# Performance work log

Measured on AMD Instinct MI355X. Metric: run time of the kernel, lower is better.

The kernel has to match this reference:

```python
import jax, jax.numpy as jnp
import numpy as np

L, H, LATENT, DM, DH, FF = 4, 4, 256, 768, 192, 1024
EPS = 1e-6      # fast_transformers RecurrentLinearAttention eps
LN_EPS = 1e-5


def make_pe(d_model=LATENT, max_len=5000):
    pos = np.arange(max_len, dtype=np.float32)[:, None]
    div = np.exp(np.arange(0, d_model, 2, dtype=np.float32) * (-np.log(10000.0) / d_model))
    pe = np.zeros((max_len, d_model), np.float32)
    pe[:, 0::2] = np.sin(pos * div)
    pe[:, 1::2] = np.cos(pos * div)
    return jnp.asarray(pe)

PE = make_pe()


def layer_norm(x, g, b):
    m = x.mean(-1, keepdims=True)
    v = ((x - m) ** 2).mean(-1, keepdims=True)
    return (x - m) * jax.lax.rsqrt(v + LN_EPS) * g + b


def setup_inputs() -> dict:
    key = jax.random.key(0)
    ks = jax.random.split(key, 16)
    bs, nj, nf, T, A, C = 8, 25, 6, 80, 6, 12
    s = 0.02
    return dict(
        x=jax.random.normal(ks[0], (bs, nj, nf, T), jnp.float32),
        y=jax.random.randint(ks[1], (bs, A), 0, C),
        ind_map=jnp.sort(jax.random.randint(ks[2], (T, bs), 0, A), axis=0),
        act_tstamps=jnp.sort(jax.random.randint(ks[3], (bs, A), 1, T + 1), axis=1).at[:, -1].set(T),
        skel_W=jax.random.normal(ks[4], (nj * nf, LATENT), jnp.float32) * s,
        skel_b=jnp.zeros((LATENT,), jnp.float32),
        muQuery=jax.random.normal(ks[5], (C, LATENT), jnp.float32),
        sigmaQuery=jax.random.normal(ks[6], (C, LATENT), jnp.float32),
        Wq=jax.random.normal(ks[7], (L, DM, DM), jnp.float32) * s,
        bq=jnp.zeros((L, DM), jnp.float32),
        Wk=jax.random.normal(ks[8], (L, DM, DM), jnp.float32) * s,
        bk=jnp.zeros((L, DM), jnp.float32),
        Wv=jax.random.normal(ks[9], (L, DM, DM), jnp.float32) * s,
        bv=jnp.zeros((L, DM), jnp.float32),
        Wo=jax.random.normal(ks[10], (L, DM, DM), jnp.float32) * s,
        bo=jnp.zeros((L, DM), jnp.float32),
        W1=jax.random.normal(ks[11], (L, DM, FF), jnp.float32) * s,
        b1=jnp.zeros((L, FF), jnp.float32),
        W2=jax.random.normal(ks[12], (L, FF, DM), jnp.float32) * s,
        b2=jnp.zeros((L, DM), jnp.float32),
        ln1_g=jnp.ones((L, DM), jnp.float32), ln1_b=jnp.zeros((L, DM), jnp.float32),
        ln2_g=jnp.ones((L, DM), jnp.float32), ln2_b=jnp.zeros((L, DM), jnp.float32),
        lnf_g=jnp.ones((DM,), jnp.float32), lnf_b=jnp.zeros((DM,), jnp.float32),
    )


def _fwd(x, y, ind_map, act_tstamps, skel_W, skel_b, muQuery, sigmaQuery,
         Wq, bq, Wk, bk, Wv, bv, Wo, bo, W1, b1, W2, b2,
         ln1_g, ln1_b, ln2_g, ln2_b, lnf_g, lnf_b):
    bs, nj, nf, T = x.shape
    # skeleton embedding: [T, bs, njoints*nfeats] @ W -> [T, bs, LATENT]
    xe = x.transpose(3, 0, 1, 2).reshape(T, bs, nj * nf) @ skel_W + skel_b
    mu_q = muQuery[y]        # [bs, A, LATENT]
    sig_q = sigmaQuery[y]
    barange = jnp.arange(bs)

    @jax.checkpoint
    def step(carry, inputs):
        S, Z = carry                         # [L,bs,H,DH,DH], [L,bs,H,DH]
        t, xt, ind_t = inputs
        cm = mu_q[barange, ind_t]            # gather per-sample current action query
        cs = sig_q[barange, ind_t]
        xseq = jnp.stack([cm, cs, xt], 0)    # [3, bs, LATENT]
        start = jnp.where(t == 0, 0, t + 2)  # PositionalEncoding(last_pos=t, offset=2)
        pe3 = jax.lax.dynamic_slice_in_dim(PE, start, 3, 0)
        xseq = xseq + pe3[:, None, :]
        h = xseq.transpose(1, 0, 2).reshape(bs, 3 * LATENT)  # flatten -> [bs, DM]
        nS, nZ = [], []
        for l in range(L):
            q = (h @ Wq[l] + bq[l]).reshape(bs, H, DH)
            k = (h @ Wk[l] + bk[l]).reshape(bs, H, DH)
            v = (h @ Wv[l] + bv[l]).reshape(bs, H, DH)
            Q = jax.nn.elu(q) + 1.0          # linear-attention feature map
            K = jax.nn.elu(k) + 1.0
            Sl = S[l] + K[..., :, None] * v[..., None, :]   # state update S += k (x) v
            Zl = Z[l] + K
            inv = 1.0 / (jnp.einsum('bhd,bhd->bh', Q, Zl) + EPS)
            att = jnp.einsum('bhd,bhdm,bh->bhm', Q, Sl, inv).reshape(bs, DM)
            h1 = layer_norm(h + att @ Wo[l] + bo[l], ln1_g[l], ln1_b[l])
            ffn = jax.nn.relu(h1 @ W1[l] + b1[l]) @ W2[l] + b2[l]
            h = layer_norm(h1 + ffn, ln2_g[l], ln2_b[l])
            nS.append(Sl); nZ.append(Zl)
        h = layer_norm(h, lnf_g, lnf_b)      # encoder final norm
        return (jnp.stack(nS), jnp.stack(nZ)), h

    S0 = jnp.zeros((L, bs, H, DH, DH), x.dtype)
    Z0 = jnp.zeros((L, bs, H, DH), x.dtype)
    _, finals = jax.lax.scan(step, (S0, Z0), (jnp.arange(T), xe, ind_map))  # finals: [T,bs,DM]
    tsel = jnp.maximum(act_tstamps - 1, 0)                       # [bs, A]
    mu = finals[:, :, :LATENT][tsel, barange[:, None]]           # [bs, A, LATENT]
    logvar = finals[:, :, LATENT:2 * LATENT][tsel, barange[:, None]]
    return mu, logvar


def reference(x, y, ind_map, act_tstamps, skel_W, skel_b, muQuery, sigmaQuery,
              Wq, bq, Wk, bk, Wv, bv, Wo, bo, W1, b1, W2, b2,
              ln1_g, ln1_b, ln2_g, ln2_b, lnf_g, lnf_b):
    return _fwd(x, y, ind_map, act_tstamps, skel_W, skel_b, muQuery, sigmaQuery,
                Wq, bq, Wk, bk, Wv, bv, Wo, bo, W1, b1, W2, b2,
                ln1_g, ln1_b, ln2_g, ln2_b, lnf_g, lnf_b)
```

## Files before the change

kernel.cpp:

```cpp
#include <hip/hip_runtime.h>
#include <math.h>

#define TT 80
#define BS 8
#define NA 6
#define DMODEL 768
#define NH 4
#define DH 192
#define FFD 1024
#define NROWS (TT*BS)
#define NQKV (3*DMODEL)

typedef __bf16 bf16;
typedef __bf16 bf16x8 __attribute__((ext_vector_type(8)));
typedef float  f32x4  __attribute__((ext_vector_type(4)));

__device__ __forceinline__ float block_reduce_sum256(float v, float* sm4) {
#pragma unroll
    for (int off = 32; off > 0; off >>= 1) v += __shfl_down(v, off, 64);
    int lane = threadIdx.x & 63, wid = threadIdx.x >> 6;
    if (lane == 0) sm4[wid] = v;
    __syncthreads();
    float r = sm4[0] + sm4[1] + sm4[2] + sm4[3];
    __syncthreads();
    return r;
}

__global__ __launch_bounds__(256) void embed_k(
        const float* __restrict__ x, const int* __restrict__ y,
        const int* __restrict__ ind_map, const float* __restrict__ skel_W,
        const float* __restrict__ skel_b, const float* __restrict__ muQ,
        const float* __restrict__ sigQ, float* __restrict__ h0,
        bf16* __restrict__ h0b) {
    __shared__ float xrow[152];
    int r = blockIdx.x;
    int t = r >> 3, b = r & 7;
    int c = threadIdx.x;
    if (c < 150) xrow[c] = x[(b * 150 + c) * TT + t];
    __syncthreads();
    float acc = skel_b[c];
    for (int jf = 0; jf < 150; jf++) acc += xrow[jf] * skel_W[jf * 256 + c];
    int ind_t = ind_map[t * 8 + b];
    int yb = y[b * NA + ind_t];
    float cm = muQ[yb * 256 + c];
    float cs = sigQ[yb * 256 + c];
    int start = (t == 0) ? 0 : (t + 2);
    float div = expf((float)(c & ~1) * (-9.210340371976184f / 256.0f));
    float p0, p1, p2;
    if (c & 1) {
        p0 = cosf((float)start * div);
        p1 = cosf((float)(start + 1) * div);
        p2 = cosf((float)(start + 2) * div);
    } else {
        p0 = sinf((float)start * div);
        p1 = sinf((float)(start + 1) * div);
        p2 = sinf((float)(start + 2) * div);
    }
    float* hr = h0 + (size_t)r * DMODEL;
    float v0 = cm + p0, v1 = cs + p1, v2 = acc + p2;
    hr[c] = v0; hr[c + 256] = v1; hr[c + 512] = v2;
    bf16* hb = h0b + (size_t)r * DMODEL;
    hb[c] = (bf16)v0; hb[c + 256] = (bf16)v1; hb[c + 512] = (bf16)v2;
}

__global__ __launch_bounds__(256) void transpose_k(
        const float* __restrict__ Wq, const float* __restrict__ Wk,
        const float* __restrict__ Wv, const float* __restrict__ Wo,
        const float* __restrict__ W1, const float* __restrict__ W2,
        bf16* __restrict__ qkvT, bf16* __restrict__ woT,
        bf16* __restrict__ w1T, bf16* __restrict__ w2T) {
    int lz = blockIdx.z;
    int l = lz >> 2, z = lz & 3;
    int K = (z == 3) ? 1024 : 768;
    int N = (z == 0) ? 2304 : (z == 2) ? 1024 : 768;
    int k0 = blockIdx.x * 32, n0 = blockIdx.y * 32;
    if (k0 >= K || n0 >= N) return;
    const float* src; bf16* dst; int ldsrc; int ncol;
    if (z == 0) {
        if (n0 < 768)       { src = Wq + (size_t)l * 768 * 768; ncol = n0; }
        else if (n0 < 1536) { src = Wk + (size_t)l * 768 * 768; ncol = n0 - 768; }
        else                { src = Wv + (size_t)l * 768 * 768; ncol = n0 - 1536; }
        dst = qkvT + (size_t)l * NQKV * DMODEL; ldsrc = 768;
    } else if (z == 1) { src = Wo + (size_t)l * 768 * 768;  dst = woT + (size_t)l * 768 * 768;  ldsrc = 768;  ncol = n0; }
    else if (z == 2)   { src = W1 + (size_t)l * 768 * 1024; dst = w1T + (size_t)l * 1024 * 768; ldsrc = 1024; ncol = n0; }
    else               { src = W2 + (size_t)l * 1024 * 768; dst = w2T + (size_t)l * 768 * 1024; ldsrc = 768;  ncol = n0; }
    __shared__ float tile[32][33];
    int tx = threadIdx.x & 31, ty = threadIdx.x >> 5;
#pragma unroll
    for (int i = 0; i < 4; i++) {
        int r = ty + 8 * i;
        tile[r][tx] = src[(size_t)(k0 + r) * ldsrc + ncol + tx];
    }
    __syncthreads();
#pragma unroll
    for (int i = 0; i < 4; i++) {
        int r = ty + 8 * i;
        dst[(size_t)(n0 + r) * K + k0 + tx] = (bf16)tile[tx][r];
    }
}

template <int EPI>
__global__ __launch_bounds__(256) void gemm_mfma(
        const bf16* __restrict__ A, const bf16* __restrict__ Bt,
        const float* __restrict__ bias_q, const float* __restrict__ bias_k,
        const float* __restrict__ bias_v, const float* __restrict__ resid,
        float* __restrict__ outF, bf16* __restrict__ outB,
        int M, int N, int K) {
    __shared__ __attribute__((aligned(16))) bf16 As0[64][40];
    __shared__ __attribute__((aligned(16))) bf16 As1[64][40];
    __shared__ __attribute__((aligned(16))) bf16 Bs0[64][40];
    __shared__ __attribute__((aligned(16))) bf16 Bs1[64][40];
    int tid = threadIdx.x;
    int m0 = blockIdx.y * 64, n0 = blockIdx.x * 64;
    int w = tid >> 6;
    int l = tid & 63;
    int lm = l & 15, lq = l >> 4;
    int sr = tid >> 2;
    int sk = (tid & 3) * 8;
    const bf16* Arow = &A[(size_t)(m0 + sr) * K];
    const bf16* Brow = &Bt[(size_t)(n0 + sr) * K];
    f32x4 acc[4] = {};
    uint4 a0 = *(const uint4*)&Arow[sk];
    uint4 a1 = *(const uint4*)&Arow[32 + sk];
    uint4 b0 = *(const uint4*)&Brow[sk];
    uint4 b1 = *(const uint4*)&Brow[32 + sk];
    for (int k0 = 0; k0 < K; k0 += 64) {
        __syncthreads();
        *(uint4*)&As0[sr][sk] = a0;
        *(uint4*)&As1[sr][sk] = a1;
        *(uint4*)&Bs0[sr][sk] = b0;
        *(uint4*)&Bs1[sr][sk] = b1;
        __syncthreads();
        int k2 = k0 + 64; if (k2 >= K) k2 = 0;
        a0 = *(const uint4*)&Arow[k2 + sk];
        a1 = *(const uint4*)&Arow[k2 + 32 + sk];
        b0 = *(const uint4*)&Brow[k2 + sk];
        b1 = *(const uint4*)&Brow[k2 + 32 + sk];
        bf16x8 af0 = *(bf16x8*)&As0[w * 16 + lm][lq * 8];
        bf16x8 af1 = *(bf16x8*)&As1[w * 16 + lm][lq * 8];
#pragma unroll
        for (int nb = 0; nb < 4; nb++) {
            bf16x8 bf0 = *(bf16x8*)&Bs0[nb * 16 + lm][lq * 8];
            acc[nb] = __builtin_amdgcn_mfma_f32_16x16x32_bf16(af0, bf0, acc[nb], 0, 0, 0);
        }
#pragma unroll
        for (int nb = 0; nb < 4; nb++) {
            bf16x8 bf1 = *(bf16x8*)&Bs1[nb * 16 + lm][lq * 8];
            acc[nb] = __builtin_amdgcn_mfma_f32_16x16x32_bf16(af1, bf1, acc[nb], 0, 0, 0);
        }
    }
#pragma unroll
    for (int nb = 0; nb < 4; nb++) {
        int col = n0 + nb * 16 + lm;
        float b;
        bool do_elu = false;
        if (EPI == 0) {
            if (col < 768)       { b = bias_q[col];        do_elu = true; }
            else if (col < 1536) { b = bias_k[col - 768];  do_elu = true; }
            else                 { b = bias_v[col - 1536]; }
        } else {
            b = bias_q[col];
        }
#pragma unroll
        for (int r = 0; r < 4; r++) {
            int row = m0 + w * 16 + lq * 4 + r;
            float v = acc[nb][r] + b;
            if (EPI == 0) {
                if (do_elu) v = (v > 0.0f) ? (v + 1.0f) : expf(v);
                outB[(size_t)row * N + col] = (bf16)v;
            } else if (EPI == 1) {
                v += resid[(size_t)row * N + col];
                outF[(size_t)row * N + col] = v;
            } else {
                v = fmaxf(v, 0.0f);
                outB[(size_t)row * N + col] = (bf16)v;
            }
        }
    }
}

__global__ __launch_bounds__(256) void ln_k(
        const float* __restrict__ in, float* __restrict__ outF,
        bf16* __restrict__ outB,
        const float* __restrict__ g, const float* __restrict__ b) {
    int wave = threadIdx.x >> 6, lane = threadIdx.x & 63;
    int row = blockIdx.x * 4 + wave;
    const float* xr = in + (size_t)row * DMODEL;
    float4 v[3];
    float s = 0.0f;
#pragma unroll
    for (int j = 0; j < 3; j++) {
        v[j] = *(const float4*)&xr[lane * 4 + 256 * j];
        s += v[j].x + v[j].y + v[j].z + v[j].w;
    }
#pragma unroll
    for (int mk = 1; mk < 64; mk <<= 1) s += __shfl_xor(s, mk, 64);
    float m = s * (1.0f / 768.0f);
    float sq = 0.0f;
#pragma unroll
    for (int j = 0; j < 3; j++) {
        v[j].x -= m; v[j].y -= m; v[j].z -= m; v[j].w -= m;
        sq += v[j].x * v[j].x + v[j].y * v[j].y + v[j].z * v[j].z + v[j].w * v[j].w;
    }
#pragma unroll
    for (int mk = 1; mk < 64; mk <<= 1) sq += __shfl_xor(sq, mk, 64);
    float r = rsqrtf(sq * (1.0f / 768.0f) + 1e-5f);
    float* orow = outF + (size_t)row * DMODEL;
    bf16* brow = outB + (size_t)row * DMODEL;
#pragma unroll
    for (int j = 0; j < 3; j++) {
        int c = lane * 4 + 256 * j;
        float4 gg = *(const float4*)&g[c];
        float4 bb = *(const float4*)&b[c];
        float o0 = v[j].x * r * gg.x + bb.x;
        float o1 = v[j].y * r * gg.y + bb.y;
        float o2 = v[j].z * r * gg.z + bb.z;
        float o3 = v[j].w * r * gg.w + bb.w;
        *(float4*)&orow[c] = make_float4(o0, o1, o2, o3);
        bf16 tmp4[4] = {(bf16)o0, (bf16)o1, (bf16)o2, (bf16)o3};
        *(uint2*)&brow[c] = *(uint2*)tmp4;
    }
}

__global__ __launch_bounds__(320) void attn_k(
        const bf16* __restrict__ qkvB, bf16* __restrict__ att) {
    __shared__ __attribute__((aligned(16))) char smem[64000];
    bf16* Qs = (bf16*)smem;
    bf16* Ks = (bf16*)(smem + 32000);
    bf16* Aij = (bf16*)smem;
    bf16* VT = (bf16*)(smem + 16640);

    int b = blockIdx.x >> 2, h = blockIdx.x & 3;
    int tid = threadIdx.x;
    int w = tid >> 6, l = tid & 63;
    int lm = l & 15, lq = l >> 4;

    uint4 vreg[6];
#pragma unroll
    for (int u = 0; u < 6; u++) {
        int c = tid + 320 * u;
        int t = c / 24, cc = c % 24;
        int d0 = cc * 8;
        size_t g = (size_t)(t * 8 + b) * NQKV + h * DH + d0;
        uint4 qv = *(const uint4*)&qkvB[g];
        uint4 kv = *(const uint4*)&qkvB[g + 768];
        vreg[u]  = *(const uint4*)&qkvB[g + 1536];
        *(uint4*)&Qs[t * 200 + d0] = qv;
        *(uint4*)&Ks[t * 200 + d0] = kv;
    }
    __syncthreads();

    f32x4 acc[5] = {};
#pragma unroll
    for (int k0 = 0; k0 < 192; k0 += 32) {
        bf16x8 af = *(bf16x8*)&Qs[(w * 16 + lm) * 200 + lq * 8 + k0];
#pragma unroll
        for (int nb = 0; nb < 5; nb++) {
            bf16x8 bfr = *(bf16x8*)&Ks[(nb * 16 + lm) * 200 + lq * 8 + k0];
            acc[nb] = __builtin_amdgcn_mfma_f32_16x16x32_bf16(af, bfr, acc[nb], 0, 0, 0);
        }
    }
    float mval[5][4];
    float rs[4] = {0.f, 0.f, 0.f, 0.f};
#pragma unroll
    for (int nb = 0; nb < 5; nb++)
#pragma unroll
        for (int r = 0; r < 4; r++) {
            int t = w * 16 + lq * 4 + r, tau = nb * 16 + lm;
            float v = (tau <= t) ? acc[nb][r] : 0.0f;
            mval[nb][r] = v;
            rs[r] += v;
        }
#pragma unroll
    for (int mk = 1; mk < 16; mk <<= 1)
#pragma unroll
        for (int r = 0; r < 4; r++) rs[r] += __shfl_xor(rs[r], mk, 64);
    float inv[4];
#pragma unroll
    for (int r = 0; r < 4; r++) inv[r] = 1.0f / (rs[r] + 1e-6f);

    __syncthreads();

#pragma unroll
    for (int nb = 0; nb < 5; nb++)
#pragma unroll
        for (int r = 0; r < 4; r++)
            Aij[(w * 16 + lq * 4 + r) * 104 + nb * 16 + lm] = (bf16)mval[nb][r];
    *(uint2*)&Aij[(tid >> 2) * 104 + 80 + (tid & 3) * 4] = make_uint2(0u, 0u);
#pragma unroll
    for (int u = 0; u < 6; u++) {
        int c = tid + 320 * u;
        int t = c / 24, cc = c % 24;
        int d0 = cc * 8;
        bf16 tmp8[8];
        *(uint4*)tmp8 = vreg[u];
#pragma unroll
        for (int j = 0; j < 8; j++) VT[(d0 + j) * 104 + t] = tmp8[j];
    }
    if (tid < 192) {
        *(uint4*)&VT[tid * 104 + 80] = make_uint4(0u, 0u, 0u, 0u);
        *(uint4*)&VT[tid * 104 + 88] = make_uint4(0u, 0u, 0u, 0u);
    }
    __syncthreads();

#pragma unroll 1
    for (int nc = 0; nc < 12; nc++) {
        f32x4 a2 = {};
#pragma unroll
        for (int k0 = 0; k0 < 96; k0 += 32) {
            bf16x8 af = *(bf16x8*)&Aij[(w * 16 + lm) * 104 + lq * 8 + k0];
            bf16x8 bfr = *(bf16x8*)&VT[(nc * 16 + lm) * 104 + lq * 8 + k0];
            a2 = __builtin_amdgcn_mfma_f32_16x16x32_bf16(af, bfr, a2, 0, 0, 0);
        }
#pragma unroll
        for (int r = 0; r < 4; r++) {
            int t = w * 16 + lq * 4 + r;
            att[(size_t)(t * 8 + b) * DMODEL + h * DH + nc * 16 + lm] =
                (bf16)(a2[r] * inv[r]);
        }
    }
}

__global__ __launch_bounds__(256) void final_k(
        const float* __restrict__ h, const int* __restrict__ act_ts,
        const float* __restrict__ g, const float* __restrict__ bb,
        float* __restrict__ out) {
    __shared__ float sm4[4];
    int ba = blockIdx.x;
    int b = ba / NA;
    int ts = act_ts[ba];
    int t = ts - 1; if (t < 0) t = 0;
    const float* xr = h + (size_t)(t * 8 + b) * DMODEL;
    int c = threadIdx.x;
    float x0 = xr[c], x1 = xr[c + 256], x2 = xr[c + 512];
    float m = block_reduce_sum256(x0 + x1 + x2, sm4) * (1.0f / 768.0f);
    float d0 = x0 - m, d1 = x1 - m, d2 = x2 - m;
    float v = block_reduce_sum256(d0 * d0 + d1 * d1 + d2 * d2, sm4) * (1.0f / 768.0f);
    float r = rsqrtf(v + 1e-5f);
    out[ba * 256 + c]            = d0 * r * g[c] + bb[c];
    out[48 * 256 + ba * 256 + c] = d1 * r * g[c + 256] + bb[c + 256];
}

extern "C" void kernel_launch(void* const* d_in, const int* in_sizes, int n_in,
                              void* d_out, int out_size, void* d_ws, size_t ws_size,
                              hipStream_t stream) {
    const float* x       = (const float*)d_in[0];
    const int*   y       = (const int*)d_in[1];
    const int*   ind_map = (const int*)d_in[2];
    const int*   act_ts  = (const int*)d_in[3];
    const float* skel_W  = (const float*)d_in[4];
    const float* skel_b  = (const float*)d_in[5];
    const float* muQ     = (const float*)d_in[6];
    const float* sigQ    = (const float*)d_in[7];
    const float* Wq = (const float*)d_in[8];   const float* bq = (const float*)d_in[9];
    const float* Wk = (const float*)d_in[10];  const float* bk = (const float*)d_in[11];
    const float* Wv = (const float*)d_in[12];  const float* bv = (const float*)d_in[13];
    const float* Wo = (const float*)d_in[14];  const float* bo = (const float*)d_in[15];
    const float* W1 = (const float*)d_in[16];  const float* b1 = (const float*)d_in[17];
    const float* W2 = (const float*)d_in[18];  const float* b2 = (const float*)d_in[19];
    const float* ln1_g = (const float*)d_in[20]; const float* ln1_b = (const float*)d_in[21];
    const float* ln2_g = (const float*)d_in[22]; const float* ln2_b = (const float*)d_in[23];
    const float* lnf_g = (const float*)d_in[24]; const float* lnf_b = (const float*)d_in[25];
    float* out = (float*)d_out;

    char* p = (char*)d_ws;
    const size_t R  = (size_t)NROWS * DMODEL;
    float* h    = (float*)p; p += R * 4;
    float* h1   = (float*)p; p += R * 4;
    float* tmp  = (float*)p; p += R * 4;
    bf16* qkvB  = (bf16*)p;  p += (size_t)NROWS * NQKV * 2;
    bf16* hB    = (bf16*)p;  p += R * 2;
    bf16* h1B   = (bf16*)p;  p += R * 2;
    bf16* attB  = (bf16*)p;  p += R * 2;
    bf16* ffn1B = (bf16*)p;  p += (size_t)NROWS * FFD * 2;
    bf16* qkvT  = (bf16*)p;  p += (size_t)4 * NQKV * DMODEL * 2;
    bf16* woT   = (bf16*)p;  p += (size_t)4 * DMODEL * DMODEL * 2;
    bf16* w1T   = (bf16*)p;  p += (size_t)4 * FFD * DMODEL * 2;
    bf16* w2T   = (bf16*)p;  p += (size_t)4 * DMODEL * FFD * 2;

    dim3 gT(32, 72, 16);
    transpose_k<<<gT, 256, 0, stream>>>(Wq, Wk, Wv, Wo, W1, W2, qkvT, woT, w1T, w2T);
    embed_k<<<NROWS, 256, 0, stream>>>(x, y, ind_map, skel_W, skel_b, muQ, sigQ, h, hB);

    dim3 gQKV(NQKV / 64, 10);
    dim3 g768(12, 10);
    dim3 g1024(16, 10);
    for (int l = 0; l < 4; l++) {
        const bf16* qkvTl = qkvT + (size_t)l * NQKV * DMODEL;
        const bf16* woTl  = woT  + (size_t)l * DMODEL * DMODEL;
        const bf16* w1Tl  = w1T  + (size_t)l * FFD * DMODEL;
        const bf16* w2Tl  = w2T  + (size_t)l * DMODEL * FFD;
        gemm_mfma<0><<<gQKV, 256, 0, stream>>>(hB, qkvTl,
                bq + l * DMODEL, bk + l * DMODEL, bv + l * DMODEL,
                nullptr, nullptr, qkvB, NROWS, NQKV, DMODEL);
        attn_k<<<32, 320, 0, stream>>>(qkvB, attB);
        gemm_mfma<1><<<g768, 256, 0, stream>>>(attB, woTl,
                bo + l * DMODEL, nullptr, nullptr, h, tmp, nullptr,
                NROWS, DMODEL, DMODEL);
        ln_k<<<NROWS / 4, 256, 0, stream>>>(tmp, h1, h1B, ln1_g + l * DMODEL, ln1_b + l * DMODEL);
        gemm_mfma<2><<<g1024, 256, 0, stream>>>(h1B, w1Tl,
                b1 + l * FFD, nullptr, nullptr, nullptr, nullptr, ffn1B,
                NROWS, FFD, DMODEL);
        gemm_mfma<1><<<g768, 256, 0, stream>>>(ffn1B, w2Tl,
                b2 + l * DMODEL, nullptr, nullptr, h1, tmp, nullptr,
                NROWS, DMODEL, FFD);
        ln_k<<<NROWS / 4, 256, 0, stream>>>(tmp, h, hB, ln2_g + l * DMODEL, ln2_b + l * DMODEL);
    }

    final_k<<<48, 256, 0, stream>>>(h, act_ts, lnf_g, lnf_b, out);
}
```

Measured before the change: 422.5 us.

## Fuse all stages into one cooperative persistent megakernel with grid barriers

Every stage (weight transpose, embedding, per-layer GEMMs, attention, layer norms, final gather) becomes a device function with grid-stride loops. They run inside a single cooperative kernel of 256 blocks separated by grid-wide syncs, with the old multi-launch path kept as a fallback. This is meant to remove the launch overhead of about 26 kernel launches. The trade-off is grid-barrier cost, a fixed grid size that may underuse or overload stages (the QKV GEMM has 360 tiles), and the attention stage now running with 256 threads instead of 320.

```diff
diff --git a/kernel.cpp b/kernel.cpp
--- a/kernel.cpp
+++ b/kernel.cpp
@@ -1,5 +1,8 @@
 #include <hip/hip_runtime.h>
+#include <hip/hip_cooperative_groups.h>
 #include <math.h>
+
+namespace cg = cooperative_groups;
 
 #define TT 80
 #define BS 8
@@ -15,287 +18,280 @@
 typedef __bf16 bf16x8 __attribute__((ext_vector_type(8)));
 typedef float  f32x4  __attribute__((ext_vector_type(4)));
 
-__device__ __forceinline__ float block_reduce_sum256(float v, float* sm4) {
-#pragma unroll
-    for (int off = 32; off > 0; off >>= 1) v += __shfl_down(v, off, 64);
-    int lane = threadIdx.x & 63, wid = threadIdx.x >> 6;
-    if (lane == 0) sm4[wid] = v;
-    __syncthreads();
-    float r = sm4[0] + sm4[1] + sm4[2] + sm4[3];
-    __syncthreads();
-    return r;
-}
-
-__global__ __launch_bounds__(256) void embed_k(
-        const float* __restrict__ x, const int* __restrict__ y,
-        const int* __restrict__ ind_map, const float* __restrict__ skel_W,
-        const float* __restrict__ skel_b, const float* __restrict__ muQ,
-        const float* __restrict__ sigQ, float* __restrict__ h0,
-        bf16* __restrict__ h0b) {
-    __shared__ float xrow[152];
-    int r = blockIdx.x;
-    int t = r >> 3, b = r & 7;
+struct MegaParams {
+    const float *x; const int *y; const int *ind_map; const int *act_ts;
+    const float *skel_W, *skel_b, *muQ, *sigQ;
+    const float *Wq, *bq, *Wk, *bk, *Wv, *bv, *Wo, *bo, *W1, *b1, *W2, *b2;
+    const float *ln1_g, *ln1_b, *ln2_g, *ln2_b, *lnf_g, *lnf_b;
+    float *out;
+    float *hF, *h1F, *tmp;
+    bf16 *qkvB, *hB, *h1B, *attB, *ffn1B, *qkvT, *woT, *w1T, *w2T;
+};
+
+__device__ void transpose_stage(const MegaParams& p, char* smem) {
+    float (*tile)[33] = (float(*)[33])smem;
+    int tx = threadIdx.x & 31, ty = threadIdx.x >> 5;
+    for (int idx = blockIdx.x; idx < 4 * 3840; idx += gridDim.x) {
+        int l = idx / 3840, r = idx % 3840;
+        int z, kt, nt, K, ldsrc;
+        if (r < 1728)      { z = 0; K = 768;  ldsrc = 768;  kt = r / 72;  nt = r % 72; }
+        else if (r < 2304) { z = 1; K = 768;  ldsrc = 768;  r -= 1728; kt = r / 24; nt = r % 24; }
+        else if (r < 3072) { z = 2; K = 768;  ldsrc = 1024; r -= 2304; kt = r / 32; nt = r % 32; }
+        else               { z = 3; K = 1024; ldsrc = 768;  r -= 3072; kt = r / 24; nt = r % 24; }
+        int k0 = kt * 32, n0 = nt * 32;
+        const float* src; bf16* dst; int ncol;
+        if (z == 0) {
+            if (n0 < 768)       { src = p.Wq + (size_t)l * 768 * 768; ncol = n0; }
+            else if (n0 < 1536) { src = p.Wk + (size_t)l * 768 * 768; ncol = n0 - 768; }
+            else                { src = p.Wv + (size_t)l * 768 * 768; ncol = n0 - 1536; }
+            dst = p.qkvT + (size_t)l * NQKV * DMODEL;
+        } else if (z == 1) { src = p.Wo + (size_t)l * 768 * 768;  dst = p.woT + (size_t)l * 768 * 768;  ncol = n0; }
+        else if (z == 2)   { src = p.W1 + (size_t)l * 768 * 1024; dst = p.w1T + (size_t)l * 1024 * 768; ncol = n0; }
+        else               { src = p.W2 + (size_t)l * 1024 * 768; dst = p.w2T + (size_t)l * 768 * 1024; ncol = n0; }
+        __syncthreads();
+#pragma unroll
+        for (int i = 0; i < 4; i++) {
+            int rr = ty + 8 * i;
+            tile[rr][tx] = src[(size_t)(k0 + rr) * ldsrc + ncol + tx];
+        }
+        __syncthreads();
+#pragma unroll
+        for (int i = 0; i < 4; i++) {
+            int rr = ty + 8 * i;
+            dst[(size_t)(n0 + rr) * K + k0 + tx] = (bf16)tile[tx][rr];
+        }
+    }
+}
+
+__device__ void embed_stage(const MegaParams& p, char* smem) {
+    float* xrow = (float*)smem;
     int c = threadIdx.x;
-    if (c < 150) xrow[c] = x[(b * 150 + c) * TT + t];
-    __syncthreads();
-    float acc = skel_b[c];
-    for (int jf = 0; jf < 150; jf++) acc += xrow[jf] * skel_W[jf * 256 + c];
-    int ind_t = ind_map[t * 8 + b];
-    int yb = y[b * NA + ind_t];
-    float cm = muQ[yb * 256 + c];
-    float cs = sigQ[yb * 256 + c];
-    int start = (t == 0) ? 0 : (t + 2);
-    float div = expf((float)(c & ~1) * (-9.210340371976184f / 256.0f));
-    float p0, p1, p2;
-    if (c & 1) {
-        p0 = cosf((float)start * div);
-        p1 = cosf((float)(start + 1) * div);
-        p2 = cosf((float)(start + 2) * div);
-    } else {
-        p0 = sinf((float)start * div);
-        p1 = sinf((float)(start + 1) * div);
-        p2 = sinf((float)(start + 2) * div);
-    }
-    float* hr = h0 + (size_t)r * DMODEL;
-    float v0 = cm + p0, v1 = cs + p1, v2 = acc + p2;
-    hr[c] = v0; hr[c + 256] = v1; hr[c + 512] = v2;
-    bf16* hb = h0b + (size_t)r * DMODEL;
-    hb[c] = (bf16)v0; hb[c + 256] = (bf16)v1; hb[c + 512] = (bf16)v2;
-}
-
-__global__ __launch_bounds__(256) void transpose_k(
-        const float* __restrict__ Wq, const float* __restrict__ Wk,
-        const float* __restrict__ Wv, const float* __restrict__ Wo,
-        const float* __restrict__ W1, const float* __restrict__ W2,
-        bf16* __restrict__ qkvT, bf16* __restrict__ woT,
-        bf16* __restrict__ w1T, bf16* __restrict__ w2T) {
-    int lz = blockIdx.z;
-    int l = lz >> 2, z = lz & 3;
-    int K = (z == 3) ? 1024 : 768;
-    int N = (z == 0) ? 2304 : (z == 2) ? 1024 : 768;
-    int k0 = blockIdx.x * 32, n0 = blockIdx.y * 32;
-    if (k0 >= K || n0 >= N) return;
-    const float* src; bf16* dst; int ldsrc; int ncol;
-    if (z == 0) {
-        if (n0 < 768)       { src = Wq + (size_t)l * 768 * 768; ncol = n0; }
-        else if (n0 < 1536) { src = Wk + (size_t)l * 768 * 768; ncol = n0 - 768; }
-        else                { src = Wv + (size_t)l * 768 * 768; ncol = n0 - 1536; }
-        dst = qkvT + (size_t)l * NQKV * DMODEL; ldsrc = 768;
-    } else if (z == 1) { src = Wo + (size_t)l * 768 * 768;  dst = woT + (size_t)l * 768 * 768;  ldsrc = 768;  ncol = n0; }
-    else if (z == 2)   { src = W1 + (size_t)l * 768 * 1024; dst = w1T + (size_t)l * 1024 * 768; ldsrc = 1024; ncol = n0; }
-    else               { src = W2 + (size_t)l * 1024 * 768; dst = w2T + (size_t)l * 768 * 1024; ldsrc = 768;  ncol = n0; }
-    __shared__ float tile[32][33];
-    int tx = threadIdx.x & 31, ty = threadIdx.x >> 5;
-#pragma unroll
-    for (int i = 0; i < 4; i++) {
-        int r = ty + 8 * i;
-        tile[r][tx] = src[(size_t)(k0 + r) * ldsrc + ncol + tx];
-    }
-    __syncthreads();
-#pragma unroll
-    for (int i = 0; i < 4; i++) {
-        int r = ty + 8 * i;
-        dst[(size_t)(n0 + r) * K + k0 + tx] = (bf16)tile[tx][r];
+    for (int r = blockIdx.x; r < NROWS; r += gridDim.x) {
+        int t = r >> 3, b = r & 7;
+        __syncthreads();
+        if (c < 150) xrow[c] = p.x[(b * 150 + c) * TT + t];
+        __syncthreads();
+        float acc = p.skel_b[c];
+        for (int jf = 0; jf < 150; jf++) acc += xrow[jf] * p.skel_W[jf * 256 + c];
+        int ind_t = p.ind_map[t * 8 + b];
+        int yb = p.y[b * NA + ind_t];
+        float cm = p.muQ[yb * 256 + c];
+        float cs = p.sigQ[yb * 256 + c];
+        int start = (t == 0) ? 0 : (t + 2);
+        float div = expf((float)(c & ~1) * (-9.210340371976184f / 256.0f));
+        float p0, p1, p2;
+        if (c & 1) {
+            p0 = cosf((float)start * div);
+            p1 = cosf((float)(start + 1) * div);
+            p2 = cosf((float)(start + 2) * div);
+        } else {
+            p0 = sinf((float)start * div);
+            p1 = sinf((float)(start + 1) * div);
+            p2 = sinf((float)(start + 2) * div);
+        }
+        float v0 = cm + p0, v1 = cs + p1, v2 = acc + p2;
+        float* hr = p.hF + (size_t)r * DMODEL;
+        hr[c] = v0; hr[c + 256] = v1; hr[c + 512] = v2;
+        bf16* hb = p.hB + (size_t)r * DMODEL;
+        hb[c] = (bf16)v0; hb[c + 256] = (bf16)v1; hb[c + 512] = (bf16)v2;
     }
 }
 
 template <int EPI>
-__global__ __launch_bounds__(256) void gemm_mfma(
-        const bf16* __restrict__ A, const bf16* __restrict__ Bt,
+__device__ void gemm_stage(const bf16* __restrict__ A, const bf16* __restrict__ Bt,
         const float* __restrict__ bias_q, const float* __restrict__ bias_k,
         const float* __restrict__ bias_v, const float* __restrict__ resid,
         float* __restrict__ outF, bf16* __restrict__ outB,
-        int M, int N, int K) {
-    __shared__ __attribute__((aligned(16))) bf16 As0[64][40];
-    __shared__ __attribute__((aligned(16))) bf16 As1[64][40];
-    __shared__ __attribute__((aligned(16))) bf16 Bs0[64][40];
-    __shared__ __attribute__((aligned(16))) bf16 Bs1[64][40];
+        int M, int N, int K, char* smem) {
+    bf16 (*As0)[40] = (bf16(*)[40])smem;
+    bf16 (*As1)[40] = (bf16(*)[40])(smem + 5120);
+    bf16 (*Bs0)[40] = (bf16(*)[40])(smem + 10240);
+    bf16 (*Bs1)[40] = (bf16(*)[40])(smem + 15360);
     int tid = threadIdx.x;
-    int m0 = blockIdx.y * 64, n0 = blockIdx.x * 64;
-    int w = tid >> 6;
-    int l = tid & 63;
+    int w = tid >> 6, l = tid & 63;
     int lm = l & 15, lq = l >> 4;
-    int sr = tid >> 2;
-    int sk = (tid & 3) * 8;
-    const bf16* Arow = &A[(size_t)(m0 + sr) * K];
-    const bf16* Brow = &Bt[(size_t)(n0 + sr) * K];
-    f32x4 acc[4] = {};
-    uint4 a0 = *(const uint4*)&Arow[sk];
-    uint4 a1 = *(const uint4*)&Arow[32 + sk];
-    uint4 b0 = *(const uint4*)&Brow[sk];
-    uint4 b1 = *(const uint4*)&Brow[32 + sk];
-    for (int k0 = 0; k0 < K; k0 += 64) {
-        __syncthreads();
-        *(uint4*)&As0[sr][sk] = a0;
-        *(uint4*)&As1[sr][sk] = a1;
-        *(uint4*)&Bs0[sr][sk] = b0;
-        *(uint4*)&Bs1[sr][sk] = b1;
-        __syncthreads();
-        int k2 = k0 + 64; if (k2 >= K) k2 = 0;
-        a0 = *(const uint4*)&Arow[k2 + sk];
-        a1 = *(const uint4*)&Arow[k2 + 32 + sk];
-        b0 = *(const uint4*)&Brow[k2 + sk];
-        b1 = *(const uint4*)&Brow[k2 + 32 + sk];
-        bf16x8 af0 = *(bf16x8*)&As0[w * 16 + lm][lq * 8];
-        bf16x8 af1 = *(bf16x8*)&As1[w * 16 + lm][lq * 8];
+    int sr = tid >> 2, sk = (tid & 3) * 8;
+    int ntn = N >> 6;
+    int ntiles = (M >> 6) * ntn;
+    for (int tile = blockIdx.x; tile < ntiles; tile += gridDim.x) {
+        int m0 = (tile / ntn) << 6, n0 = (tile % ntn) << 6;
+        const bf16* Arow = &A[(size_t)(m0 + sr) * K];
+        const bf16* Brow = &Bt[(size_t)(n0 + sr) * K];
+        f32x4 acc[4] = {};
+        uint4 a0 = *(const uint4*)&Arow[sk];
+        uint4 a1 = *(const uint4*)&Arow[32 + sk];
+        uint4 b0 = *(const uint4*)&Brow[sk];
+        uint4 b1 = *(const uint4*)&Brow[32 + sk];
+        for (int k0 = 0; k0 < K; k0 += 64) {
+            __syncthreads();
+            *(uint4*)&As0[sr][sk] = a0;
+            *(uint4*)&As1[sr][sk] = a1;
+            *(uint4*)&Bs0[sr][sk] = b0;
+            *(uint4*)&Bs1[sr][sk] = b1;
+            __syncthreads();
+            int k2 = k0 + 64; if (k2 >= K) k2 = 0;
+            a0 = *(const uint4*)&Arow[k2 + sk];
+            a1 = *(const uint4*)&Arow[k2 + 32 + sk];
+            b0 = *(const uint4*)&Brow[k2 + sk];
+            b1 = *(const uint4*)&Brow[k2 + 32 + sk];
+            bf16x8 af0 = *(bf16x8*)&As0[w * 16 + lm][lq * 8];
+            bf16x8 af1 = *(bf16x8*)&As1[w * 16 + lm][lq * 8];
+#pragma unroll
+            for (int nb = 0; nb < 4; nb++) {
+                bf16x8 bf0 = *(bf16x8*)&Bs0[nb * 16 + lm][lq * 8];
+                acc[nb] = __builtin_amdgcn_mfma_f32_16x16x32_bf16(af0, bf0, acc[nb], 0, 0, 0);
+            }
+#pragma unroll
+            for (int nb = 0; nb < 4; nb++) {
+                bf16x8 bf1 = *(bf16x8*)&Bs1[nb * 16 + lm][lq * 8];
+                acc[nb] = __builtin_amdgcn_mfma_f32_16x16x32_bf16(af1, bf1, acc[nb], 0, 0, 0);
+            }
+        }
 #pragma unroll
         for (int nb = 0; nb < 4; nb++) {
-            bf16x8 bf0 = *(bf16x8*)&Bs0[nb * 16 + lm][lq * 8];
-            acc[nb] = __builtin_amdgcn_mfma_f32_16x16x32_bf16(af0, bf0, acc[nb], 0, 0, 0);
-        }
-#pragma unroll
-        for (int nb = 0; nb < 4; nb++) {
-            bf16x8 bf1 = *(bf16x8*)&Bs1[nb * 16 + lm][lq * 8];
-            acc[nb] = __builtin_amdgcn_mfma_f32_16x16x32_bf16(af1, bf1, acc[nb], 0, 0, 0);
-        }
-    }
-#pragma unroll
-    for (int nb = 0; nb < 4; nb++) {
-        int col = n0 + nb * 16 + lm;
-        float b;
-        bool do_elu = false;
-        if (EPI == 0) {
-            if (col < 768)       { b = bias_q[col];        do_elu = true; }
-            else if (col < 1536) { b = bias_k[col - 768];  do_elu = true; }
-            else                 { b = bias_v[col - 1536]; }
-        } else {
-            b = bias_q[col];
-        }
-#pragma unroll
-        for (int r = 0; r < 4; r++) {
-            int row = m0 + w * 16 + lq * 4 + r;
-            float v = acc[nb][r] + b;
+            int col = n0 + nb * 16 + lm;
+            float b;
+            bool do_elu = false;
             if (EPI == 0) {
-                if (do_elu) v = (v > 0.0f) ? (v + 1.0f) : expf(v);
-                outB[(size_t)row * N + col] = (bf16)v;
-            } else if (EPI == 1) {
-                v += resid[(size_t)row * N + col];
-                outF[(size_t)row * N + col] = v;
+                if (col < 768)       { b = bias_q[col];        do_elu = true; }
+                else if (col < 1536) { b = bias_k[col - 768];  do_elu = true; }
+                else                 { b = bias_v[col - 1536]; }
             } else {
-                v = fmaxf(v, 0.0f);
-                outB[(size_t)row * N + col] = (bf16)v;
-            }
-        }
-    }
-}
-
-__global__ __launch_bounds__(256) void ln_k(
-        const float* __restrict__ in, float* __restrict__ outF,
-        bf16* __restrict__ outB,
-        const float* __restrict__ g, const float* __restrict__ b) {
+                b = bias_q[col];
+            }
+#pragma unroll
+            for (int r = 0; r < 4; r++) {
+                int row = m0 + w * 16 + lq * 4 + r;
+                float v = acc[nb][r] + b;
+                if (EPI == 0) {
+                    if (do_elu) v = (v > 0.0f) ? (v + 1.0f) : expf(v);
+                    outB[(size_t)row * N + col] = (bf16)v;
+                } else if (EPI == 1) {
+                    v += resid[(size_t)row * N + col];
+                    outF[(size_t)row * N + col] = v;
+                } else {
+                    v = fmaxf(v, 0.0f);
+                    outB[(size_t)row * N + col] = (bf16)v;
+                }
+            }
+        }
+    }
+}
+
+__device__ void ln_stage(const float* __restrict__ in, float* __restrict__ outF,
+        bf16* __restrict__ outB, const float* __restrict__ g,
+        const float* __restrict__ b) {
     int wave = threadIdx.x >> 6, lane = threadIdx.x & 63;
-    int row = blockIdx.x * 4 + wave;
-    const float* xr = in + (size_t)row * DMODEL;
-    float4 v[3];
-    float s = 0.0f;
-#pragma unroll
-    for (int j = 0; j < 3; j++) {
-        v[j] = *(const float4*)&xr[lane * 4 + 256 * j];
-        s += v[j].x + v[j].y + v[j].z + v[j].w;
-    }
-#pragma unroll
-    for (int mk = 1; mk < 64; mk <<= 1) s += __shfl_xor(s, mk, 64);
-    float m = s * (1.0f / 768.0f);
-    float sq = 0.0f;
-#pragma unroll
-    for (int j = 0; j < 3; j++) {
-        v[j].x -= m; v[j].y -= m; v[j].z -= m; v[j].w -= m;
-        sq += v[j].x * v[j].x + v[j].y * v[j].y + v[j].z * v[j].z + v[j].w * v[j].w;
-    }
-#pragma unroll
-    for (int mk = 1; mk < 64; mk <<= 1) sq += __shfl_xor(sq, mk, 64);
-    float r = rsqrtf(sq * (1.0f / 768.0f) + 1e-5f);
-    float* orow = outF + (size_t)row * DMODEL;
-    bf16* brow = outB + (size_t)row * DMODEL;
-#pragma unroll
-    for (int j = 0; j < 3; j++) {
-        int c = lane * 4 + 256 * j;
-        float4 gg = *(const float4*)&g[c];
-        float4 bb = *(const float4*)&b[c];
-        float o0 = v[j].x * r * gg.x + bb.x;
-        float o1 = v[j].y * r * gg.y + bb.y;
-        float o2 = v[j].z * r * gg.z + bb.z;
-        float o3 = v[j].w * r * gg.w + bb.w;
-        *(float4*)&orow[c] = make_float4(o0, o1, o2, o3);
-        bf16 tmp4[4] = {(bf16)o0, (bf16)o1, (bf16)o2, (bf16)o3};
-        *(uint2*)&brow[c] = *(uint2*)tmp4;
-    }
-}
-
-__global__ __launch_bounds__(320) void attn_k(
-        const bf16* __restrict__ qkvB, bf16* __restrict__ att) {
-    __shared__ __attribute__((aligned(16))) char smem[64000];
-    bf16* Qs = (bf16*)smem;
-    bf16* Ks = (bf16*)(smem + 32000);
+    for (int row = blockIdx.x * 4 + wave; row < NROWS; row += gridDim.x * 4) {
+        const float* xr = in + (size_t)row * DMODEL;
+        float4 v[3];
+        float s = 0.0f;
+#pragma unroll
+        for (int j = 0; j < 3; j++) {
+            v[j] = *(const float4*)&xr[lane * 4 + 256 * j];
+            s += v[j].x + v[j].y + v[j].z + v[j].w;
+        }
+#pragma unroll
+        for (int mk = 1; mk < 64; mk <<= 1) s += __shfl_xor(s, mk, 64);
+        float m = s * (1.0f / 768.0f);
+        float sq = 0.0f;
+#pragma unroll
+        for (int j = 0; j < 3; j++) {
+            v[j].x -= m; v[j].y -= m; v[j].z -= m; v[j].w -= m;
+            sq += v[j].x * v[j].x + v[j].y * v[j].y + v[j].z * v[j].z + v[j].w * v[j].w;
+        }
+#pragma unroll
+        for (int mk = 1; mk < 64; mk <<= 1) sq += __shfl_xor(sq, mk, 64);
+        float r = rsqrtf(sq * (1.0f / 768.0f) + 1e-5f);
+        float* orow = outF + (size_t)row * DMODEL;
+        bf16* brow = outB + (size_t)row * DMODEL;
+#pragma unroll
+        for (int j = 0; j < 3; j++) {
+            int c = lane * 4 + 256 * j;
+            float4 gg = *(const float4*)&g[c];
+            float4 bb = *(const float4*)&b[c];
+            float o0 = v[j].x * r * gg.x + bb.x;
+            float o1 = v[j].y * r * gg.y + bb.y;
+            float o2 = v[j].z * r * gg.z + bb.z;
+            float o3 = v[j].w * r * gg.w + bb.w;
+            *(float4*)&orow[c] = make_float4(o0, o1, o2, o3);
+            bf16 t4[4] = {(bf16)o0, (bf16)o1, (bf16)o2, (bf16)o3};
+            *(uint2*)&brow[c] = *(uint2*)t4;
+        }
+    }
+}
+
+__device__ void attn_stage(const bf16* __restrict__ qkvB, bf16* __restrict__ att,
+                           char* smem) {
+    if (blockIdx.x >= 32) return;
+    bf16* Qs  = (bf16*)smem;
+    bf16* Ks  = (bf16*)(smem + 32000);
     bf16* Aij = (bf16*)smem;
-    bf16* VT = (bf16*)(smem + 16640);
-
+    bf16* VT  = (bf16*)(smem + 16640);
     int b = blockIdx.x >> 2, h = blockIdx.x & 3;
     int tid = threadIdx.x;
     int w = tid >> 6, l = tid & 63;
     int lm = l & 15, lq = l >> 4;
 
-    uint4 vreg[6];
-#pragma unroll
-    for (int u = 0; u < 6; u++) {
-        int c = tid + 320 * u;
-        int t = c / 24, cc = c % 24;
-        int d0 = cc * 8;
+    for (int c = tid; c < 1920; c += 256) {
+        int t = c / 24, d0 = (c % 24) * 8;
         size_t g = (size_t)(t * 8 + b) * NQKV + h * DH + d0;
-        uint4 qv = *(const uint4*)&qkvB[g];
-        uint4 kv = *(const uint4*)&qkvB[g + 768];
-        vreg[u]  = *(const uint4*)&qkvB[g + 1536];
-        *(uint4*)&Qs[t * 200 + d0] = qv;
-        *(uint4*)&Ks[t * 200 + d0] = kv;
-    }
-    __syncthreads();
-
-    f32x4 acc[5] = {};
-#pragma unroll
-    for (int k0 = 0; k0 < 192; k0 += 32) {
-        bf16x8 af = *(bf16x8*)&Qs[(w * 16 + lm) * 200 + lq * 8 + k0];
-#pragma unroll
-        for (int nb = 0; nb < 5; nb++) {
-            bf16x8 bfr = *(bf16x8*)&Ks[(nb * 16 + lm) * 200 + lq * 8 + k0];
-            acc[nb] = __builtin_amdgcn_mfma_f32_16x16x32_bf16(af, bfr, acc[nb], 0, 0, 0);
-        }
-    }
-    float mval[5][4];
-    float rs[4] = {0.f, 0.f, 0.f, 0.f};
-#pragma unroll
-    for (int nb = 0; nb < 5; nb++)
-#pragma unroll
-        for (int r = 0; r < 4; r++) {
-            int t = w * 16 + lq * 4 + r, tau = nb * 16 + lm;
-            float v = (tau <= t) ? acc[nb][r] : 0.0f;
-            mval[nb][r] = v;
-            rs[r] += v;
-        }
-#pragma unroll
-    for (int mk = 1; mk < 16; mk <<= 1)
-#pragma unroll
-        for (int r = 0; r < 4; r++) rs[r] += __shfl_xor(rs[r], mk, 64);
-    float inv[4];
-#pragma unroll
-    for (int r = 0; r < 4; r++) inv[r] = 1.0f / (rs[r] + 1e-6f);
-
-    __syncthreads();
-
-#pragma unroll
-    for (int nb = 0; nb < 5; nb++)
-#pragma unroll
-        for (int r = 0; r < 4; r++)
-            Aij[(w * 16 + lq * 4 + r) * 104 + nb * 16 + lm] = (bf16)mval[nb][r];
-    *(uint2*)&Aij[(tid >> 2) * 104 + 80 + (tid & 3) * 4] = make_uint2(0u, 0u);
-#pragma unroll
-    for (int u = 0; u < 6; u++) {
-        int c = tid + 320 * u;
-        int t = c / 24, cc = c % 24;
-        int d0 = cc * 8;
-        bf16 tmp8[8];
-        *(uint4*)tmp8 = vreg[u];
-#pragma unroll
-        for (int j = 0; j < 8; j++) VT[(d0 + j) * 104 + t] = tmp8[j];
+        *(uint4*)&Qs[t * 200 + d0] = *(const uint4*)&qkvB[g];
+        *(uint4*)&Ks[t * 200 + d0] = *(const uint4*)&qkvB[g + 768];
+    }
+    __syncthreads();
+
+    float mval[2][5][4];
+    float inv[2][4];
+    int nrt = (w == 0) ? 2 : 1;
+    for (int i = 0; i < nrt; i++) {
+        int rt = w + i * 4;
+        f32x4 acc[5] = {};
+#pragma unroll
+        for (int k0 = 0; k0 < 192; k0 += 32) {
+            bf16x8 af = *(bf16x8*)&Qs[(rt * 16 + lm) * 200 + lq * 8 + k0];
+#pragma unroll
+            for (int nb = 0; nb < 5; nb++) {
+                bf16x8 bfr = *(bf16x8*)&Ks[(nb * 16 + lm) * 200 + lq * 8 + k0];
+                acc[nb] = __builtin_amdgcn_mfma_f32_16x16x32_bf16(af, bfr, acc[nb], 0, 0, 0);
+            }
+        }
+        float rs[4] = {0.f, 0.f, 0.f, 0.f};
+#pragma unroll
+        for (int nb = 0; nb < 5; nb++)
+#pragma unroll
+            for (int r = 0; r < 4; r++) {
+                int t = rt * 16 + lq * 4 + r, tau = nb * 16 + lm;
+                float v = (tau <= t) ? acc[nb][r] : 0.0f;
+                mval[i][nb][r] = v;
+                rs[r] += v;
+            }
+#pragma unroll
+        for (int mk = 1; mk < 16; mk <<= 1)
+#pragma unroll
+            for (int r = 0; r < 4; r++) rs[r] += __shfl_xor(rs[r], mk, 64);
+#pragma unroll
+        for (int r = 0; r < 4; r++) inv[i][r] = 1.0f / (rs[r] + 1e-6f);
+    }
+    __syncthreads();
+
+    for (int i = 0; i < nrt; i++) {
+        int rt = w + i * 4;
+#pragma unroll
+        for (int nb = 0; nb < 5; nb++)
+#pragma unroll
+            for (int r = 0; r < 4; r++)
+                Aij[(rt * 16 + lq * 4 + r) * 104 + nb * 16 + lm] = (bf16)mval[i][nb][r];
+    }
+    for (int c2 = tid; c2 < 320; c2 += 256)
+        *(uint2*)&Aij[(c2 >> 2) * 104 + 80 + (c2 & 3) * 4] = make_uint2(0u, 0u);
+    for (int c = tid; c < 1920; c += 256) {
+        int t = c / 24, d0 = (c % 24) * 8;
+        uint4 vv = *(const uint4*)&qkvB[(size_t)(t * 8 + b) * NQKV + h * DH + 1536 + d0];
+        bf16 t8[8];
+        *(uint4*)t8 = vv;
+#pragma unroll
+        for (int j = 0; j < 8; j++) VT[(d0 + j) * 104 + t] = t8[j];
     }
     if (tid < 192) {
         *(uint4*)&VT[tid * 104 + 80] = make_uint4(0u, 0u, 0u, 0u);
@@ -303,109 +299,190 @@
     }
     __syncthreads();
 
+    for (int i = 0; i < nrt; i++) {
+        int rt = w + i * 4;
 #pragma unroll 1
-    for (int nc = 0; nc < 12; nc++) {
-        f32x4 a2 = {};
-#pragma unroll
-        for (int k0 = 0; k0 < 96; k0 += 32) {
-            bf16x8 af = *(bf16x8*)&Aij[(w * 16 + lm) * 104 + lq * 8 + k0];
-            bf16x8 bfr = *(bf16x8*)&VT[(nc * 16 + lm) * 104 + lq * 8 + k0];
-            a2 = __builtin_amdgcn_mfma_f32_16x16x32_bf16(af, bfr, a2, 0, 0, 0);
-        }
-#pragma unroll
-        for (int r = 0; r < 4; r++) {
-            int t = w * 16 + lq * 4 + r;
-            att[(size_t)(t * 8 + b) * DMODEL + h * DH + nc * 16 + lm] =
-                (bf16)(a2[r] * inv[r]);
-        }
-    }
-}
-
-__global__ __launch_bounds__(256) void final_k(
-        const float* __restrict__ h, const int* __restrict__ act_ts,
-        const float* __restrict__ g, const float* __restrict__ bb,
-        float* __restrict__ out) {
-    __shared__ float sm4[4];
+        for (int nc = 0; nc < 12; nc++) {
+            f32x4 a2 = {};
+#pragma unroll
+            for (int k0 = 0; k0 < 96; k0 += 32) {
+                bf16x8 af  = *(bf16x8*)&Aij[(rt * 16 + lm) * 104 + lq * 8 + k0];
+                bf16x8 bfr = *(bf16x8*)&VT[(nc * 16 + lm) * 104 + lq * 8 + k0];
+                a2 = __builtin_amdgcn_mfma_f32_16x16x32_bf16(af, bfr, a2, 0, 0, 0);
+            }
+#pragma unroll
+            for (int r = 0; r < 4; r++) {
+                int t = rt * 16 + lq * 4 + r;
+                att[(size_t)(t * 8 + b) * DMODEL + h * DH + nc * 16 + lm] =
+                    (bf16)(a2[r] * inv[i][r]);
+            }
+        }
+    }
+}
+
+__device__ void final_stage(const MegaParams& p, char* smem) {
+    if (blockIdx.x >= 48) return;
+    float* sm4 = (float*)smem;
     int ba = blockIdx.x;
     int b = ba / NA;
-    int ts = act_ts[ba];
+    int ts = p.act_ts[ba];
     int t = ts - 1; if (t < 0) t = 0;
-    const float* xr = h + (size_t)(t * 8 + b) * DMODEL;
+    const float* xr = p.hF + (size_t)(t * 8 + b) * DMODEL;
     int c = threadIdx.x;
+    int lane = c & 63, wid = c >> 6;
     float x0 = xr[c], x1 = xr[c + 256], x2 = xr[c + 512];
-    float m = block_reduce_sum256(x0 + x1 + x2, sm4) * (1.0f / 768.0f);
+    float s = x0 + x1 + x2;
+#pragma unroll
+    for (int off = 32; off > 0; off >>= 1) s += __shfl_down(s, off, 64);
+    if (lane == 0) sm4[wid] = s;
+    __syncthreads();
+    float m = (sm4[0] + sm4[1] + sm4[2] + sm4[3]) * (1.0f / 768.0f);
+    __syncthreads();
     float d0 = x0 - m, d1 = x1 - m, d2 = x2 - m;
-    float v = block_reduce_sum256(d0 * d0 + d1 * d1 + d2 * d2, sm4) * (1.0f / 768.0f);
+    float q = d0 * d0 + d1 * d1 + d2 * d2;
+#pragma unroll
+    for (int off = 32; off > 0; off >>= 1) q += __shfl_down(q, off, 64);
+    if (lane == 0) sm4[wid] = q;
+    __syncthreads();
+    float v = (sm4[0] + sm4[1] + sm4[2] + sm4[3]) * (1.0f / 768.0f);
     float r = rsqrtf(v + 1e-5f);
-    out[ba * 256 + c]            = d0 * r * g[c] + bb[c];
-    out[48 * 256 + ba * 256 + c] = d1 * r * g[c + 256] + bb[c + 256];
+    p.out[ba * 256 + c]            = d0 * r * p.lnf_g[c] + p.lnf_b[c];
+    p.out[48 * 256 + ba * 256 + c] = d1 * r * p.lnf_g[c + 256] + p.lnf_b[c + 256];
+}
+
+__global__ __launch_bounds__(256) void mega(MegaParams p) {
+    __shared__ __attribute__((aligned(16))) char smem[64000];
+    cg::grid_group grid = cg::this_grid();
+
+    transpose_stage(p, smem);
+    embed_stage(p, smem);
+    grid.sync();
+
+    for (int l = 0; l < 4; l++) {
+        const bf16* qkvTl = p.qkvT + (size_t)l * NQKV * DMODEL;
+        const bf16* woTl  = p.woT  + (size_t)l * DMODEL * DMODEL;
+        const bf16* w1Tl  = p.w1T  + (size_t)l * FFD * DMODEL;
+        const bf16* w2Tl  = p.w2T  + (size_t)l * DMODEL * FFD;
+        gemm_stage<0>(p.hB, qkvTl, p.bq + l * DMODEL, p.bk + l * DMODEL,
+                      p.bv + l * DMODEL, nullptr, nullptr, p.qkvB,
+                      NROWS, NQKV, DMODEL, smem);
+        grid.sync();
+        attn_stage(p.qkvB, p.attB, smem);
+        grid.sync();
+        gemm_stage<1>(p.attB, woTl, p.bo + l * DMODEL, nullptr, nullptr,
+                      p.hF, p.tmp, nullptr, NROWS, DMODEL, DMODEL, smem);
+        grid.sync();
+        ln_stage(p.tmp, p.h1F, p.h1B, p.ln1_g + l * DMODEL, p.ln1_b + l * DMODEL);
+        grid.sync();
+        gemm_stage<2>(p.h1B, w1Tl, p.b1 + l * FFD, nullptr, nullptr,
+                      nullptr, nullptr, p.ffn1B, NROWS, FFD, DMODEL, smem);
+        grid.sync();
+        gemm_stage<1>(p.ffn1B, w2Tl, p.b2 + l * DMODEL, nullptr, nullptr,
+                      p.h1F, p.tmp, nullptr, NROWS, DMODEL, FFD, smem);
+        grid.sync();
+        ln_stage(p.tmp, p.hF, p.hB, p.ln2_g + l * DMODEL, p.ln2_b + l * DMODEL);
+        grid.sync();
+    }
+
+    final_stage(p, smem);
+}
+
+__global__ __launch_bounds__(256) void transpose_wrap(MegaParams p) {
+    __shared__ __attribute__((aligned(16))) char smem[4352];
+    transpose_stage(p, smem);
+}
+__global__ __launch_bounds__(256) void embed_wrap(MegaParams p) {
+    __shared__ __attribute__((aligned(16))) char smem[640];
+    embed_stage(p, smem);
+}
+template <int EPI>
+__global__ __launch_bounds__(256) void gemm_wrap(
+        const bf16* A, const bf16* Bt, const float* bq, const float* bk,
+        const float* bv, const float* resid, float* outF, bf16* outB,
+        int M, int N, int K) {
+    __shared__ __attribute__((aligned(16))) char smem[20480];
+    gemm_stage<EPI>(A, Bt, bq, bk, bv, resid, outF, outB, M, N, K, smem);
+}
+__global__ __launch_bounds__(256) void attn_wrap(const bf16* qkvB, bf16* att) {
+    __shared__ __attribute__((aligned(16))) char smem[64000];
+    attn_stage(qkvB, att, smem);
+}
+__global__ __launch_bounds__(256) void ln_wrap(const float* in, float* outF,
+        bf16* outB, const float* g, const float* b) {
+    ln_stage(in, outF, outB, g, b);
+}
+__global__ __launch_bounds__(256) void final_wrap(MegaParams p) {
+    __shared__ __attribute__((aligned(16))) char smem[64];
+    final_stage(p, smem);
 }
 
 extern "C" void kernel_launch(void* const* d_in, const int* in_sizes, int n_in,
                               void* d_out, int out_size, void* d_ws, size_t ws_size,
                               hipStream_t stream) {
-    const float* x       = (const float*)d_in[0];
-    const int*   y       = (const int*)d_in[1];
-    const int*   ind_map = (const int*)d_in[2];
-    const int*   act_ts  = (const int*)d_in[3];
-    const float* skel_W  = (const float*)d_in[4];
-    const float* skel_b  = (const float*)d_in[5];
-    const float* muQ     = (const float*)d_in[6];
-    const float* sigQ    = (const float*)d_in[7];
-    const float* Wq = (const float*)d_in[8];   const float* bq = (const float*)d_in[9];
-    const float* Wk = (const float*)d_in[10];  const float* bk = (const float*)d_in[11];
-    const float* Wv = (const float*)d_in[12];  const float* bv = (const float*)d_in[13];
-    const float* Wo = (const float*)d_in[14];  const float* bo = (const float*)d_in[15];
-    const float* W1 = (const float*)d_in[16];  const float* b1 = (const float*)d_in[17];
-    const float* W2 = (const float*)d_in[18];  const float* b2 = (const float*)d_in[19];
-    const float* ln1_g = (const float*)d_in[20]; const float* ln1_b = (const float*)d_in[21];
-    const float* ln2_g = (const float*)d_in[22]; const float* ln2_b = (const float*)d_in[23];
-    const float* lnf_g = (const float*)d_in[24]; const float* lnf_b = (const float*)d_in[25];
-    float* out = (float*)d_out;
+    MegaParams prm;
+    prm.x       = (const float*)d_in[0];
+    prm.y       = (const int*)d_in[1];
+    prm.ind_map = (const int*)d_in[2];
+    prm.act_ts  = (const int*)d_in[3];
+    prm.skel_W  = (const float*)d_in[4];
+    prm.skel_b  = (const float*)d_in[5];
+    prm.muQ     = (const float*)d_in[6];
+    prm.sigQ    = (const float*)d_in[7];
+    prm.Wq = (const float*)d_in[8];   prm.bq = (const float*)d_in[9];
+    prm.Wk = (const float*)d_in[10];  prm.bk = (const float*)d_in[11];
+    prm.Wv = (const float*)d_in[12];  prm.bv = (const float*)d_in[13];
+    prm.Wo = (const float*)d_in[14];  prm.bo = (const float*)d_in[15];
+    prm.W1 = (const float*)d_in[16];  prm.b1 = (const float*)d_in[17];
+    prm.W2 = (const float*)d_in[18];  prm.b2 = (const float*)d_in[19];
+    prm.ln1_g = (const float*)d_in[20]; prm.ln1_b = (const float*)d_in[21];
+    prm.ln2_g = (const float*)d_in[22]; prm.ln2_b = (const float*)d_in[23];
+    prm.lnf_g = (const float*)d_in[24]; prm.lnf_b = (const float*)d_in[25];
+    prm.out = (float*)d_out;
 
     char* p = (char*)d_ws;
-    const size_t R  = (size_t)NROWS * DMODEL;
-    float* h    = (float*)p; p += R * 4;
-    float* h1   = (float*)p; p += R * 4;
-    float* tmp  = (float*)p; p += R * 4;
-    bf16* qkvB  = (bf16*)p;  p += (size_t)NROWS * NQKV * 2;
-    bf16* hB    = (bf16*)p;  p += R * 2;
-    bf16* h1B   = (bf16*)p;  p += R * 2;
-    bf16* attB  = (bf16*)p;  p += R * 2;
-    bf16* ffn1B = (bf16*)p;  p += (size_t)NROWS * FFD * 2;
-    bf16* qkvT  = (bf16*)p;  p += (size_t)4 * NQKV * DMODEL * 2;
-    bf16* woT   = (bf16*)p;  p += (size_t)4 * DMODEL * DMODEL * 2;
-    bf16* w1T   = (bf16*)p;  p += (size_t)4 * FFD * DMODEL * 2;
-    bf16* w2T   = (bf16*)p;  p += (size_t)4 * DMODEL * FFD * 2;
-
-    dim3 gT(32, 72, 16);
-    transpose_k<<<gT, 256, 0, stream>>>(Wq, Wk, Wv, Wo, W1, W2, qkvT, woT, w1T, w2T);
-    embed_k<<<NROWS, 256, 0, stream>>>(x, y, ind_map, skel_W, skel_b, muQ, sigQ, h, hB);
-
-    dim3 gQKV(NQKV / 64, 10);
-    dim3 g768(12, 10);
-    dim3 g1024(16, 10);
-    for (int l = 0; l < 4; l++) {
-        const bf16* qkvTl = qkvT + (size_t)l * NQKV * DMODEL;
-        const bf16* woTl  = woT  + (size_t)l * DMODEL * DMODEL;
-        const bf16* w1Tl  = w1T  + (size_t)l * FFD * DMODEL;
-        const bf16* w2Tl  = w2T  + (size_t)l * DMODEL * FFD;
-        gemm_mfma<0><<<gQKV, 256, 0, stream>>>(hB, qkvTl,
-                bq + l * DMODEL, bk + l * DMODEL, bv + l * DMODEL,
-                nullptr, nullptr, qkvB, NROWS, NQKV, DMODEL);
-        attn_k<<<32, 320, 0, stream>>>(qkvB, attB);
-        gemm_mfma<1><<<g768, 256, 0, stream>>>(attB, woTl,
-                bo + l * DMODEL, nullptr, nullptr, h, tmp, nullptr,
-                NROWS, DMODEL, DMODEL);
-        ln_k<<<NROWS / 4, 256, 0, stream>>>(tmp, h1, h1B, ln1_g + l * DMODEL, ln1_b + l * DMODEL);
-        gemm_mfma<2><<<g1024, 256, 0, stream>>>(h1B, w1Tl,
-                b1 + l * FFD, nullptr, nullptr, nullptr, nullptr, ffn1B,
-                NROWS, FFD, DMODEL);
-        gemm_mfma<1><<<g768, 256, 0, stream>>>(ffn1B, w2Tl,
-                b2 + l * DMODEL, nullptr, nullptr, h1, tmp, nullptr,
-                NROWS, DMODEL, FFD);
-        ln_k<<<NROWS / 4, 256, 0, stream>>>(tmp, h, hB, ln2_g + l * DMODEL, ln2_b + l * DMODEL);
-    }
-
-    final_k<<<48, 256, 0, stream>>>(h, act_ts, lnf_g, lnf_b, out);
-}
+    const size_t R = (size_t)NROWS * DMODEL;
+    prm.hF    = (float*)p; p += R * 4;
+    prm.h1F   = (float*)p; p += R * 4;
+    prm.tmp   = (float*)p; p += R * 4;
+    prm.qkvB  = (bf16*)p;  p += (size_t)NROWS * NQKV * 2;
+    prm.hB    = (bf16*)p;  p += R * 2;
+    prm.h1B   = (bf16*)p;  p += R * 2;
+    prm.attB  = (bf16*)p;  p += R * 2;
+    prm.ffn1B = (bf16*)p;  p += (size_t)NROWS * FFD * 2;
+    prm.qkvT  = (bf16*)p;  p += (size_t)4 * NQKV * DMODEL * 2;
+    prm.woT   = (bf16*)p;  p += (size_t)4 * DMODEL * DMODEL * 2;
+    prm.w1T   = (bf16*)p;  p += (size_t)4 * FFD * DMODEL * 2;
+    prm.w2T   = (bf16*)p;  p += (size_t)4 * DMODEL * FFD * 2;
+
+    void* kargs[] = { (void*)&prm };
+    hipError_t err = hipLaunchCooperativeKernel((const void*)mega, dim3(256),
+                                                dim3(256), kargs, 0, stream);
+    if (err != hipSuccess) {
+        transpose_wrap<<<512, 256, 0, stream>>>(prm);
+        embed_wrap<<<NROWS, 256, 0, stream>>>(prm);
+        for (int l = 0; l < 4; l++) {
+            const bf16* qkvTl = prm.qkvT + (size_t)l * NQKV * DMODEL;
+            const bf16* woTl  = prm.woT  + (size_t)l * DMODEL * DMODEL;
+            const bf16* w1Tl  = prm.w1T  + (size_t)l * FFD * DMODEL;
+            const bf16* w2Tl  = prm.w2T  + (size_t)l * DMODEL * FFD;
+            gemm_wrap<0><<<360, 256, 0, stream>>>(prm.hB, qkvTl,
+                    prm.bq + l * DMODEL, prm.bk + l * DMODEL, prm.bv + l * DMODEL,
+                    nullptr, nullptr, prm.qkvB, NROWS, NQKV, DMODEL);
+            attn_wrap<<<32, 256, 0, stream>>>(prm.qkvB, prm.attB);
+            gemm_wrap<1><<<120, 256, 0, stream>>>(prm.attB, woTl,
+                    prm.bo + l * DMODEL, nullptr, nullptr, prm.hF,
+                    prm.tmp, nullptr, NROWS, DMODEL, DMODEL);
+            ln_wrap<<<160, 256, 0, stream>>>(prm.tmp, prm.h1F, prm.h1B,
+                    prm.ln1_g + l * DMODEL, prm.ln1_b + l * DMODEL);
+            gemm_wrap<2><<<160, 256, 0, stream>>>(prm.h1B, w1Tl,
+                    prm.b1 + l * FFD, nullptr, nullptr, nullptr,
+                    nullptr, prm.ffn1B, NROWS, FFD, DMODEL);
+            gemm_wrap<1><<<120, 256, 0, stream>>>(prm.ffn1B, w2Tl,
+                    prm.b2 + l * DMODEL, nullptr, nullptr, prm.h1F,
+                    prm.tmp, nullptr, NROWS, DMODEL, FFD);
+            ln_wrap<<<160, 256, 0, stream>>>(prm.tmp, prm.hF, prm.hB,
+                    prm.ln2_g + l * DMODEL, prm.ln2_b + l * DMODEL);
+        }
+        final_wrap<<<48, 256, 0, stream>>>(prm);
+    }
+}
```

After: 1.333 ms. 3.16x slower.
